# Optimization experiments

Measured on AMD Instinct MI355X. Metric: run time of the kernel, lower is better.

Reference implementation:

```python
import jax, jax.numpy as jnp
import numpy as np
from jax import lax

C = 256
POOL = 7
NUM_CLASSES = 81
D = NUM_CLASSES - 1
STRIDES = (4, 8, 16, 32)
DEC_MULT = (0.1, 0.1, 0.2, 0.2)  # decode_settings: multipliers on raw deltas
LOG_MAX = float(np.log(1000.0 / 16.0))


def setup_inputs() -> dict:
    key = jax.random.key(0)
    ks = jax.random.split(key, 16)
    n, Rp = 2, 512
    R = n * Rp
    img = 800.0
    cx = jax.random.uniform(ks[0], (R,), minval=0.0, maxval=img)
    cy = jax.random.uniform(ks[1], (R,), minval=0.0, maxval=img)
    w = jax.random.uniform(ks[2], (R,), minval=16.0, maxval=300.0)
    h = jax.random.uniform(ks[3], (R,), minval=16.0, maxval=300.0)
    x1 = jnp.clip(cx - w / 2, 0.0, img - 1.0)
    y1 = jnp.clip(cy - h / 2, 0.0, img - 1.0)
    x2 = jnp.minimum(jnp.maximum(cx + w / 2, x1 + 1.0), img)
    y2 = jnp.minimum(jnp.maximum(cy + h / 2, y1 + 1.0), img)
    proposals = jnp.stack([x1, y1, x2, y2], -1)
    imidx = jnp.repeat(jnp.arange(n, dtype=jnp.int32), Rp)
    fmaps = {}
    for li, s in enumerate(STRIDES):
        hw = int(800 // s)
        fmaps[f"fmap{li}"] = jax.random.normal(ks[4 + li], (n, hw, hw, C), jnp.float32)
    c1, clin = C * POOL * POOL, 1024
    def lin(k, fi, fo):
        return (jax.random.normal(k, (fi, fo), jnp.float32) / np.sqrt(fi).astype(np.float32),
                jnp.zeros((fo,), jnp.float32))
    W0, b0 = lin(ks[8], c1, clin)
    W1, b1 = lin(ks[9], clin, clin)
    Wc, bc = lin(ks[10], clin, NUM_CLASSES)
    Wr, br = lin(ks[11], clin, NUM_CLASSES * 4)
    imsizes = jnp.full((n, 2), img, jnp.float32)  # (h, w) per image
    return dict(proposals=proposals, imidx=imidx, **fmaps,
                W0=W0, b0=b0, W1=W1, b1=b1, Wc=Wc, bc=bc, Wr=Wr, br=br,
                imsizes=imsizes, score_thr=0.05, iou_thr=0.5, imtop=100, min_size=1.0)


def _roi_align_level(fmap, boxes, imidx, stride):
    # fmap [n,H,W,C], boxes [R,4] xyxy in image coords; 1 sample per bin, bilinear.
    n, H, W, c = fmap.shape
    s = 1.0 / stride
    x1, y1, x2, y2 = boxes[:, 0] * s, boxes[:, 1] * s, boxes[:, 2] * s, boxes[:, 3] * s
    g = (jnp.arange(POOL, dtype=jnp.float32) + 0.5) / POOL  # bin centers in [0,1]
    xs = x1[:, None] + g[None, :] * (x2 - x1)[:, None] - 0.5  # [R,POOL]
    ys = y1[:, None] + g[None, :] * (y2 - y1)[:, None] - 0.5
    R = boxes.shape[0]
    xx = jnp.broadcast_to(xs[:, None, :], (R, POOL, POOL))
    yy = jnp.broadcast_to(ys[:, :, None], (R, POOL, POOL))
    x0f, y0f = jnp.floor(xx), jnp.floor(yy)
    wx, wy = xx - x0f, yy - y0f
    x0 = jnp.clip(x0f.astype(jnp.int32), 0, W - 1)
    x1i = jnp.clip(x0f.astype(jnp.int32) + 1, 0, W - 1)
    y0 = jnp.clip(y0f.astype(jnp.int32), 0, H - 1)
    y1i = jnp.clip(y0f.astype(jnp.int32) + 1, 0, H - 1)
    ii = imidx[:, None, None]
    v00 = fmap[ii, y0, x0]; v01 = fmap[ii, y0, x1i]
    v10 = fmap[ii, y1i, x0]; v11 = fmap[ii, y1i, x1i]  # each [R,POOL,POOL,C]
    wx, wy = wx[..., None], wy[..., None]
    return (v00 * (1 - wx) * (1 - wy) + v01 * wx * (1 - wy)
            + v10 * (1 - wx) * wy + v11 * wx * wy)


def _forward(proposals, imidx, fmaps, W0, b0, W1, b1, Wc, bc, Wr, br,
             imsizes, score_thr, iou_thr, imtop, min_size):
    R = proposals.shape[0]
    pw = proposals[:, 2] - proposals[:, 0]
    ph = proposals[:, 3] - proposals[:, 1]
    # FPN level assignment (torchvision canonical formula)
    lvl = jnp.floor(4.0 + jnp.log2(jnp.sqrt(pw * ph) / 224.0 + 1e-6))
    lvl = jnp.clip(lvl, 2, 5).astype(jnp.int32) - 2
    pooled = jnp.zeros((R, POOL, POOL, C), fmaps[0].dtype)
    for k, (fm, st) in enumerate(zip(fmaps, STRIDES)):
        pk = _roi_align_level(fm, proposals, imidx, st)
        pooled = jnp.where((lvl == k)[:, None, None, None], pk, pooled)
    # two-FC head + cls/reg
    x = pooled.reshape(R, -1)
    x = jax.nn.relu(x @ W0 + b0)
    x = jax.nn.relu(x @ W1 + b1)
    reg = (x @ Wr + br).reshape(R, NUM_CLASSES, 4)[:, 1:]      # [R,D,4]
    scr = jax.nn.softmax(x @ Wc + bc, axis=-1)[:, 1:]          # [R,D]
    cls = jnp.broadcast_to(jnp.arange(1, NUM_CLASSES, dtype=jnp.int32), (R, D))
    # decode boxes (proposal cwh + weighted deltas, log-space clamp)
    cx = (proposals[:, 0] + proposals[:, 2]) * 0.5
    cy = (proposals[:, 1] + proposals[:, 3]) * 0.5
    dx = reg[..., 0] * DEC_MULT[0]
    dy = reg[..., 1] * DEC_MULT[1]
    dw = jnp.minimum(reg[..., 2] * DEC_MULT[2], LOG_MAX)
    dh = jnp.minimum(reg[..., 3] * DEC_MULT[3], LOG_MAX)
    ncx = dx * pw[:, None] + cx[:, None]
    ncy = dy * ph[:, None] + cy[:, None]
    nw = jnp.exp(dw) * pw[:, None]
    nh = jnp.exp(dh) * ph[:, None]
    hb = imsizes[imidx, 0][:, None]
    wb = imsizes[imidx, 1][:, None]
    bx1 = jnp.clip(ncx - nw / 2, 0.0, wb); bx2 = jnp.clip(ncx + nw / 2, 0.0, wb)
    by1 = jnp.clip(ncy - nh / 2, 0.0, hb); by2 = jnp.clip(ncy + nh / 2, 0.0, hb)
    boxes = jnp.stack([bx1, by1, bx2, by2], -1)                # [R,D,4]
    valid = (scr > score_thr) & (bx2 - bx1 >= min_size) & (by2 - by1 >= min_size)
    # flatten roi-class pairs; class-offset boxes = torchvision batched_nms trick
    M = R * D
    boxes_f = boxes.reshape(M, 4)
    scr_f = scr.reshape(M)
    cls_f = cls.reshape(M)
    valid_f = valid.reshape(M)
    imidx_f = jnp.repeat(imidx, D)
    off = cls_f.astype(boxes_f.dtype)[:, None] * (jnp.max(imsizes) + 2.0)
    bo = boxes_f + off
    areas = (bo[:, 2] - bo[:, 0]) * (bo[:, 3] - bo[:, 1])
    def nms(scores0):
        def step(scores, _):
            i = jnp.argmax(scores)
            s = scores[i]
            b = bo[i]
            iw = jnp.clip(jnp.minimum(b[2], bo[:, 2]) - jnp.maximum(b[0], bo[:, 0]), 0.0)
            ih = jnp.clip(jnp.minimum(b[3], bo[:, 3]) - jnp.maximum(b[1], bo[:, 1]), 0.0)
            inter = iw * ih
            iou = inter / (areas[i] + areas - inter + 1e-6)
            scores = jnp.where(iou > iou_thr, -1.0, scores)
            scores = scores.at[i].set(-1.0)
            return scores, (i, s)
        _, (idx, s) = lax.scan(step, scores0, None, length=imtop)
        return idx, s
    n = imsizes.shape[0]
    ob, osc, ocl = [], [], []
    for i in range(n):
        s0 = jnp.where(valid_f & (imidx_f == i), scr_f, -1.0)
        idx, s = nms(s0)
        keep = s > 0.0  # padded slots have score <= 0
        ob.append(jnp.where(keep[:, None], boxes_f[idx], 0.0))
        osc.append(jnp.where(keep, s, 0.0))
        ocl.append(jnp.where(keep, cls_f[idx], -1))
    return jnp.stack(ob), jnp.stack(osc), jnp.stack(ocl)


def reference(proposals, imidx, fmap0, fmap1, fmap2, fmap3, W0, b0, W1, b1,
              Wc, bc, Wr, br, imsizes, score_thr, iou_thr, imtop, min_size):
    return _forward(proposals, imidx, (fmap0, fmap1, fmap2, fmap3), W0, b0, W1,
                    b1, Wc, bc, Wr, br, imsizes, score_thr, iou_thr, int(imtop),
                    min_size)
```

## Files before the change

kernel.cpp:

```cpp
#include <hip/hip_runtime.h>
#include <math.h>

#define CCH 256
#define NPOOL 7
#define NCLS 81
#define DCLS 80
#define NHEAD 512
#define FLOG_MAX 4.1351666f

typedef _Float16 half8 __attribute__((ext_vector_type(8)));
typedef _Float16 half4 __attribute__((ext_vector_type(4)));
typedef float floatx4 __attribute__((ext_vector_type(4)));

__global__ void zero_k(float4* __restrict__ p, int count4)
{
    int i = blockIdx.x * blockDim.x + threadIdx.x;
    if (i < count4) p[i] = make_float4(0.f, 0.f, 0.f, 0.f);
}

__device__ __forceinline__ void roi_setup(
    const float* __restrict__ prop, const int* __restrict__ imidx,
    const float* __restrict__ f0, const float* __restrict__ f1,
    const float* __restrict__ f2, const float* __restrict__ f3,
    int h0, int h1, int h2, int h3, int b,
// ... 87 lines not shown
    half4 h, l;
#pragma unroll
    for (int e = 0; e < 4; ++e) {
        float v = p00[e] * w00 + p01[e] * w01 + p10[e] * w10 + p11[e] * w11;
        _Float16 hh = (_Float16)v;
        h[e] = hh;
        l[e] = (_Float16)(v - (float)hh);
    }
    size_t idx = (size_t)b * CCH + c4;
    *(half4*)(poolH + idx) = h;
    *(half4*)(poolL + idx) = l;
}

__device__ __forceinline__ void conv_fast_body(
    const float* __restrict__ W, _Float16* __restrict__ WtH,
    _Float16* __restrict__ WtL, int K, int N, int k0, int n0, int t,
    float (*sh)[65])
{
#pragma unroll
    for (int p = 0; p < 4; ++p) {
        int idx = p * 256 + t;
        int kr = idx >> 4, nc = (idx & 15) * 4;
        float4 v = *(const float4*)(W + (size_t)(k0 + kr) * N + n0 + nc);
        sh[kr][nc + 0] = v.x; sh[kr][nc + 1] = v.y;
        sh[kr][nc + 2] = v.z; sh[kr][nc + 3] = v.w;
    }
    __syncthreads();
#pragma unroll
    for (int p = 0; p < 4; ++p) {
        int idx = p * 256 + t;
        int nr = idx >> 4, kc = (idx & 15) * 4;
        half4 h, l;
#pragma unroll
        for (int i = 0; i < 4; ++i) {
            float v = sh[kc + i][nr];
            _Float16 hh = (_Float16)v;
            h[i] = hh;
            l[i] = (_Float16)(v - (float)hh);
        }
        *(half4*)(WtH + (size_t)(n0 + nr) * K + k0 + kc) = h;
        *(half4*)(WtL + (size_t)(n0 + nr) * K + k0 + kc) = l;
    }
}

__device__ __forceinline__ void conv_guard_body(
    const float* __restrict__ W, _Float16* __restrict__ WtH,
    _Float16* __restrict__ WtL, int K, int N, int Kt, int rowofs,
    int k0, int n0, int t, float (*sh)[65])
{
#pragma unroll
    for (int p = 0; p < 4; ++p) {
        int idx = p * 256 + t;
        int kr = idx >> 4, nc = (idx & 15) * 4;
#pragma unroll
        for (int e = 0; e < 4; ++e) {
            int nn = n0 + nc + e;
            sh[kr][nc + e] = (nn < N) ? W[(size_t)(k0 + kr) * N + nn] : 0.0f;
        }
    }
    __syncthreads();
#pragma unroll
    for (int p = 0; p < 4; ++p) {
        int idx = p * 256 + t;
        int nr = idx >> 4, kc = (idx & 15) * 4;
        if (n0 + nr < N) {
            half4 h, l;
#pragma unroll
            for (int i = 0; i < 4; ++i) {
                float v = sh[kc + i][nr];
                _Float16 hh = (_Float16)v;
                h[i] = hh;
                l[i] = (_Float16)(v - (float)hh);
            }
            *(half4*)(WtH + (size_t)(rowofs + n0 + nr) * Kt + k0 + kc) = h;
            *(half4*)(WtL + (size_t)(rowofs + n0 + nr) * Kt + k0 + kc) = l;
        }
    }
}

__global__ __launch_bounds__(256) void pre_uber_k(
    const float* __restrict__ prop, const int* __restrict__ imidx,
    const float* __restrict__ f0, const float* __restrict__ f1,
    const float* __restrict__ f2, const float* __restrict__ f3,
    int h0, int h1, int h2, int h3,
    _Float16* __restrict__ poolH, _Float16* __restrict__ poolL,
    const float* __restrict__ W0, _Float16* __restrict__ W0tH, _Float16* __restrict__ W0tL,
    float4* __restrict__ zp, int zc4,
    int* __restrict__ cntp, int ncnt,
    int R, int K0, int CL)
{
    __shared__ float sh[64][65];
    int b = blockIdx.x, t = threadIdx.x;

    if (blockIdx.x == 0 && t < ncnt) cntp[t] = 0;

    int NB_ROI = (R * 49) / 4;
    int KT0 = K0 / 64, NT0 = CL / 64;
    int NB_CW0 = KT0 * NT0;

    if (b < NB_ROI) {
        roi_f16v4_body(prop, imidx, f0, f1, f2, f3, h0, h1, h2, h3, b, t,
                       poolH, poolL);
        return;
    }
    b -= NB_ROI;
    if (b < NB_CW0) {
        int k0 = (b % KT0) * 64, n0 = (b / KT0) * 64;
        conv_fast_body(W0, W0tH, W0tL, K0, CL, k0, n0, t, sh);
        return;
    }
    b -= NB_CW0;
    {
        int i = b * 256 + t;
        if (i < zc4) zp[i] = make_float4(0.f, 0.f, 0.f, 0.f);
    }
}

__global__ void act_split_k(const float* __restrict__ acc,
                            const float* __restrict__ bias,
                            _Float16* __restrict__ outH,
                            _Float16* __restrict__ outL,
                            int total, int CL)
{
    int i = (blockIdx.x * blockDim.x + threadIdx.x) * 4;
    if (i >= total) return;
    int b = i % CL;
    float4 v = *(const float4*)(acc + i);
    float4 bb = *(const float4*)(bias + b);
    const float* pv = (const float*)&v;
    const float* pb = (const float*)&bb;
    half4 h, l;
#pragma unroll
    for (int e = 0; e < 4; ++e) {
        float f = fmaxf(pv[e] + pb[e], 0.0f);
        _Float16 hh = (_Float16)f;
        h[e] = hh;
        l[e] = (_Float16)(f - (float)hh);
    }
    *(half4*)(outH + i) = h;
    *(half4*)(outL + i) = l;
}

__device__ __forceinline__ void dma16(const _Float16* g, _Float16* l)
{
    __builtin_amdgcn_global_load_lds(
        (const __attribute__((address_space(1))) unsigned int*)g,
        (__attribute__((address_space(3))) unsigned int*)l, 16, 0, 0);
}

#define LDKE 32
#define DKQ_SWZ(lane)  ((((lane) & 3) ^ (((lane) >> 3) & 3)) << 3)
#define FK_SWZ(lane)   (((((lane) >> 4) ^ (((lane) >> 1) & 3))) << 3)

__global__ __launch_bounds__(256) void gemm_fc0_conv_k(
    const _Float16* __restrict__ Ah, const _Float16* __restrict__ Al,
    const _Float16* __restrict__ Bh, const _Float16* __restrict__ Bl,
    float* __restrict__ Cacc, int M, int N, int K, int Kc, int SP, int nbg,
    const float* __restrict__ W1, _Float16* __restrict__ W1tH, _Float16* __restrict__ W1tL,
    const float* __restrict__ Wc, const float* __restrict__ Wr,
    _Float16* __restrict__ WheadtH, _Float16* __restrict__ WheadtL, int CL)
{
    __shared__ __align__(16) char smem[4 * 128 * LDKE * 2];

    int t = threadIdx.x;

    if (blockIdx.x >= nbg) {
        float (*sh)[65] = (float(*)[65])smem;
        int b = blockIdx.x - nbg;
        int KT1 = CL / 64;
        int NB_CW1 = KT1 * KT1;
        int NB_CWc = KT1 * ((NCLS + 63) / 64);
        if (b < NB_CW1) {
            int k0 = (b % KT1) * 64, n0 = (b / KT1) * 64;
            conv_fast_body(W1, W1tH, W1tL, CL, CL, k0, n0, t, sh);
            return;
        }
        b -= NB_CW1;
        if (b < NB_CWc) {
            int k0 = (b % KT1) * 64, n0 = (b / KT1) * 64;
            conv_guard_body(Wc, WheadtH, WheadtL, CL, NCLS, CL, 0, k0, n0, t, sh);
            return;
        }
        b -= NB_CWc;
        {
            int k0 = (b % KT1) * 64, n0 = (b / KT1) * 64;
            conv_guard_body(Wr, WheadtH, WheadtL, CL, NCLS * 4, CL, NCLS, k0, n0, t, sh);
            return;
        }
    }

    _Float16* sAh = (_Float16*)smem;
    _Float16* sAl = sAh + 128 * LDKE;
    _Float16* sBh = sAl + 128 * LDKE;
    _Float16* sBl = sBh + 128 * LDKE;

    int bid = blockIdx.x;
    int z = bid % SP;
    int q = bid / SP;
    int NT = N >> 7;
    int nn = q % NT;
    int m = q / NT;
    int m0 = m * 128, n0 = nn * 128;
    int kb = z * Kc;
    int ke = min(K, kb + Kc);

    int lane = t & 63, w = t >> 6;
    int wr = w >> 1, wc = w & 1;
    int fr = lane & 15;
    int fk = FK_SWZ(lane);

    int drow = w * 32 + (lane >> 2);
    int dkq = DKQ_SWZ(lane);
    const _Float16* gAh = Ah + (size_t)(m0 + drow) * K + dkq;
    const _Float16* gAl = Al + (size_t)(m0 + drow) * K + dkq;
    const _Float16* gBh = Bh + (size_t)(n0 + drow) * K + dkq;
    const _Float16* gBl = Bl + (size_t)(n0 + drow) * K + dkq;
    size_t rowskip = (size_t)16 * K;

    _Float16* lAh0 = &sAh[(w * 2 + 0) * 512];
    _Float16* lAh1 = &sAh[(w * 2 + 1) * 512];
    _Float16* lAl0 = &sAl[(w * 2 + 0) * 512];
    _Float16* lAl1 = &sAl[(w * 2 + 1) * 512];
    _Float16* lBh0 = &sBh[(w * 2 + 0) * 512];
    _Float16* lBh1 = &sBh[(w * 2 + 1) * 512];
    _Float16* lBl0 = &sBl[(w * 2 + 0) * 512];
    _Float16* lBl1 = &sBl[(w * 2 + 1) * 512];

    floatx4 acc[4][4] = {};

    for (int k0 = kb; k0 < ke; k0 += 32) {
        dma16(gAh + k0, lAh0);
        dma16(gAh + rowskip + k0, lAh1);
        dma16(gAl + k0, lAl0);
        dma16(gAl + rowskip + k0, lAl1);
        dma16(gBh + k0, lBh0);
        dma16(gBh + rowskip + k0, lBh1);
        dma16(gBl + k0, lBl0);
        dma16(gBl + rowskip + k0, lBl1);
        __syncthreads();

        half8 ah[4], al[4], bh[4], bl[4];
#pragma unroll
        for (int i = 0; i < 4; ++i) {
            int ar = wr * 64 + i * 16 + fr;
            ah[i] = *(const half8*)&sAh[ar * LDKE + fk];
            al[i] = *(const half8*)&sAl[ar * LDKE + fk];
            int bc = wc * 64 + i * 16 + fr;
            bh[i] = *(const half8*)&sBh[bc * LDKE + fk];
            bl[i] = *(const half8*)&sBl[bc * LDKE + fk];
        }
#pragma unroll
        for (int i = 0; i < 4; ++i)
#pragma unroll
            for (int j = 0; j < 4; ++j) {
                acc[i][j] = __builtin_amdgcn_mfma_f32_16x16x32_f16(ah[i], bh[j], acc[i][j], 0, 0, 0);
                acc[i][j] = __builtin_amdgcn_mfma_f32_16x16x32_f16(ah[i], bl[j], acc[i][j], 0, 0, 0);
                acc[i][j] = __builtin_amdgcn_mfma_f32_16x16x32_f16(al[i], bh[j], acc[i][j], 0, 0, 0);
            }
        __syncthreads();
    }

    int rbase = (lane >> 4) * 4;
#pragma unroll
    for (int i = 0; i < 4; ++i)
#pragma unroll
        for (int j = 0; j < 4; ++j) {
            int col = n0 + wc * 64 + j * 16 + fr;
#pragma unroll
            for (int r = 0; r < 4; ++r) {
                int row = m0 + wr * 64 + i * 16 + rbase + r;
                atomicAdd(&Cacc[(size_t)row * N + col], acc[i][j][r]);
            }
        }
}

__global__ __launch_bounds__(256) void gemm_mfma_fused64_k(
    const _Float16* __restrict__ Ah, const _Float16* __restrict__ Al,
    const _Float16* __restrict__ Bh, const _Float16* __restrict__ Bl,
    const float* __restrict__ bias,
    float* __restrict__ Cout,
    _Float16* __restrict__ outH, _Float16* __restrict__ outL,
    int M, int N, int K, int mode)
{
    __shared__ _Float16 sAh[2][64 * LDKE], sAl[2][64 * LDKE];
    __shared__ _Float16 sBh[2][64 * LDKE], sBl[2][64 * LDKE];

    int m0 = blockIdx.y * 64, n0 = blockIdx.x * 64;
    int t = threadIdx.x;
    int lane = t & 63, w = t >> 6;
    int wr = w >> 1, wc = w & 1;
    int fr = lane & 15;
    int fk = FK_SWZ(lane);

    int drow = w * 16 + (lane >> 2);
    int dkq = DKQ_SWZ(lane);
    const _Float16* gAh = Ah + (size_t)(m0 + drow) * K + dkq;
    const _Float16* gAl = Al + (size_t)(m0 + drow) * K + dkq;
    const _Float16* gBh = Bh + (size_t)(n0 + drow) * K + dkq;
    const _Float16* gBl = Bl + (size_t)(n0 + drow) * K + dkq;
    int lofs = w * 512;

    int nt = K >> 5;

    dma16(gAh + 0, &sAh[0][lofs]);
    dma16(gAl + 0, &sAl[0][lofs]);
    dma16(gBh + 0, &sBh[0][lofs]);
    dma16(gBl + 0, &sBl[0][lofs]);
    __syncthreads();

    floatx4 acc[2][2] = {};

    for (int tt = 0; tt < nt; ++tt) {
        int c = tt & 1, nb = c ^ 1;
        if (tt + 1 < nt) {
            int k1 = (tt + 1) << 5;
            dma16(gAh + k1, &sAh[nb][lofs]);
            dma16(gAl + k1, &sAl[nb][lofs]);
            dma16(gBh + k1, &sBh[nb][lofs]);
            dma16(gBl + k1, &sBl[nb][lofs]);
        }

        half8 ah[2], av[2], bh[2], bv[2];
#pragma unroll
        for (int i = 0; i < 2; ++i) {
            int ar = wr * 32 + i * 16 + fr;
            ah[i] = *(const half8*)&sAh[c][ar * LDKE + fk];
            av[i] = *(const half8*)&sAl[c][ar * LDKE + fk];
            int bc = wc * 32 + i * 16 + fr;
            bh[i] = *(const half8*)&sBh[c][bc * LDKE + fk];
            bv[i] = *(const half8*)&sBl[c][bc * LDKE + fk];
        }
#pragma unroll
        for (int i = 0; i < 2; ++i)
#pragma unroll
            for (int j = 0; j < 2; ++j) {
                acc[i][j] = __builtin_amdgcn_mfma_f32_16x16x32_f16(ah[i], bh[j], acc[i][j], 0, 0, 0);
                acc[i][j] = __builtin_amdgcn_mfma_f32_16x16x32_f16(ah[i], bv[j], acc[i][j], 0, 0, 0);
                acc[i][j] = __builtin_amdgcn_mfma_f32_16x16x32_f16(av[i], bh[j], acc[i][j], 0, 0, 0);
            }
        __syncthreads();
    }

    int rbase = (lane >> 4) * 4;
#pragma unroll
    for (int i = 0; i < 2; ++i)
#pragma unroll
        for (int j = 0; j < 2; ++j) {
            int col = n0 + wc * 32 + j * 16 + fr;
#pragma unroll
            for (int r = 0; r < 4; ++r) {
                int row = m0 + wr * 32 + i * 16 + rbase + r;
                float v = acc[i][j][r];
                if (mode == 0) {
                    Cout[(size_t)row * N + col] = v;
                } else {
                    float f = fmaxf(v + bias[col], 0.0f);
                    _Float16 hh = (_Float16)f;
                    outH[(size_t)row * N + col] = hh;
                    outL[(size_t)row * N + col] = (_Float16)(f - (float)hh);
                }
            }
        }
}

__global__ __launch_bounds__(256) void gemm_splitk_k(const float* __restrict__ A,
                                                     const float* __restrict__ B,
                                                     const float* __restrict__ abias,
                                                     float* __restrict__ Cacc,
                                                     int M, int N, int K, int Kc)
{
    __shared__ float Ast[16][68];
    __shared__ float Bs[16][68];

    int m0 = blockIdx.y * 64, n0 = blockIdx.x * 64;
    int kb = blockIdx.z * Kc;
    int ke = min(K, kb + Kc);
    int tid = threadIdx.x;
    int tx = tid & 15, ty = tid >> 4;
    int arow = tid >> 2, akq = (tid & 3) << 2;
    int bcol = tid & 63, bk = tid >> 6;

    const float* Arow = A + (size_t)(m0 + arow) * K;
    bool nfull = (n0 + 64 <= N);

    float acc[4][4] = {};

    for (int k0 = kb; k0 < ke; k0 += 16) {
        float4 av = *(const float4*)(Arow + k0 + akq);
        if (abias) {
            av.x = fmaxf(av.x + abias[k0 + akq + 0], 0.0f);
            av.y = fmaxf(av.y + abias[k0 + akq + 1], 0.0f);
            av.z = fmaxf(av.z + abias[k0 + akq + 2], 0.0f);
            av.w = fmaxf(av.w + abias[k0 + akq + 3], 0.0f);
        }
        float bv[4];
        if (nfull) {
#pragma unroll
            for (int e = 0; e < 4; ++e)
                bv[e] = B[(size_t)(k0 + bk * 4 + e) * N + n0 + bcol];
        } else {
            bool ok = (n0 + bcol) < N;
#pragma unroll
            for (int e = 0; e < 4; ++e)
                bv[e] = ok ? B[(size_t)(k0 + bk * 4 + e) * N + n0 + bcol] : 0.0f;
        }
        __syncthreads();
        Ast[akq + 0][arow] = av.x;
        Ast[akq + 1][arow] = av.y;
        Ast[akq + 2][arow] = av.z;
        Ast[akq + 3][arow] = av.w;
#pragma unroll
        for (int e = 0; e < 4; ++e) Bs[bk * 4 + e][bcol] = bv[e];
        __syncthreads();

#pragma unroll
        for (int kk = 0; kk < 16; ++kk) {
            float4 af = *(const float4*)&Ast[kk][ty * 4];
            float4 bf = *(const float4*)&Bs[kk][tx * 4];
            float a_[4] = {af.x, af.y, af.z, af.w};
            float b_[4] = {bf.x, bf.y, bf.z, bf.w};
#pragma unroll
            for (int i = 0; i < 4; ++i)
#pragma unroll
                for (int j = 0; j < 4; ++j)
                    acc[i][j] = fmaf(a_[i], b_[j], acc[i][j]);
        }
    }

#pragma unroll
    for (int i = 0; i < 4; ++i) {
        int row = m0 + ty * 4 + i;
#pragma unroll
        for (int j = 0; j < 4; ++j) {
            int col = n0 + tx * 4 + j;
            if (col < N) atomicAdd(&Cacc[(size_t)row * N + col], acc[i][j]);
        }
    }
}

__global__ void softmax_k(const float* __restrict__ logits, int ldl,
                          const float* __restrict__ bc,
                          float* __restrict__ scr)
{
    int r = blockIdx.x;
    int t = threadIdx.x;
    const float* row = logits + (size_t)r * ldl;

    float v0 = row[t] + bc[t];
    float v1 = (t + 64 < NCLS) ? (row[t + 64] + bc[t + 64]) : -INFINITY;
    float m = fmaxf(v0, v1);
#pragma unroll
    for (int o = 32; o > 0; o >>= 1) m = fmaxf(m, __shfl_down(m, o));
    m = __shfl(m, 0);

    float e0 = expf(v0 - m);
    float e1 = (t + 64 < NCLS) ? expf(v1 - m) : 0.0f;
    float sum = e0 + e1;
#pragma unroll
    for (int o = 32; o > 0; o >>= 1) sum += __shfl_down(sum, o);
    sum = __shfl(sum, 0);
    float inv = 1.0f / sum;

    if (t >= 1)        scr[(size_t)r * DCLS + (t - 1)]  = e0 * inv;
    if (t + 64 < NCLS) scr[(size_t)r * DCLS + (t + 63)] = e1 * inv;
}

__global__ __launch_bounds__(256) void compact_k(
    const float* __restrict__ head, int ldh, int regofs,
    const float* __restrict__ bc,
    const float* __restrict__ br,
    const float* __restrict__ prop,
    const int* __restrict__ imidx,
    const float* __restrict__ imsz,
    const float* __restrict__ score_thr_p,
    const float* __restrict__ min_size_p,
    int* __restrict__ cntp,
    int* __restrict__ cidx,
    float* __restrict__ cscore,
    float* __restrict__ cbo,
    float* __restrict__ cbox,
    float* __restrict__ carea,
    int M, int n, int R)
{
    int wid = threadIdx.x >> 6, t = threadIdx.x & 63;
    int r = blockIdx.x * 4 + wid;
    if (r >= R) return;

    const float* row = head + (size_t)r * ldh;
    float v0 = row[t] + bc[t];
    float v1 = (t + 64 < NCLS) ? (row[t + 64] + bc[t + 64]) : -INFINITY;
    float m = fmaxf(v0, v1);
#pragma unroll
    for (int o = 32; o > 0; o >>= 1) m = fmaxf(m, __shfl_down(m, o));
    m = __shfl(m, 0);

    float e0 = expf(v0 - m);
    float e1 = (t + 64 < NCLS) ? expf(v1 - m) : 0.0f;
    float sum = e0 + e1;
#pragma unroll
    for (int o = 32; o > 0; o >>= 1) sum += __shfl_down(sum, o);
    sum = __shfl(sum, 0);
    float inv = 1.0f / sum;

    float score_thr = score_thr_p[0];
    float min_size  = min_size_p[0];
    float immax = imsz[0];
    for (int q = 1; q < 2 * n; ++q) immax = fmaxf(immax, imsz[q]);

    int img = imidx[r];
    int base = img * M;
    const float* pr = prop + (size_t)r * 4;
    float pw = pr[2] - pr[0], ph = pr[3] - pr[1];
    float cx = (pr[0] + pr[2]) * 0.5f, cy = (pr[1] + pr[3]) * 0.5f;
// ... 314 lines not shown
        float bx1 = fminf(fmaxf(ncx - nw * 0.5f, 0.0f), wbound);
        float bx2 = fminf(fmaxf(ncx + nw * 0.5f, 0.0f), wbound);
        float by1 = fminf(fmaxf(ncy - nh * 0.5f, 0.0f), hbound);
        float by2 = fminf(fmaxf(ncy + nh * 0.5f, 0.0f), hbound);
        if (bx2 - bx1 < min_size || by2 - by1 < min_size) continue;

        float off = (float)cls * (immax + 2.0f);
        int p = atomicAdd(&cnt, 1);
        cidx[base + p] = j;
        cscore[base + p] = s;
        cbox[(size_t)(base + p) * 4 + 0] = bx1;
        cbox[(size_t)(base + p) * 4 + 1] = by1;
        cbox[(size_t)(base + p) * 4 + 2] = bx2;
        cbox[(size_t)(base + p) * 4 + 3] = by2;
        cbo[(size_t)(base + p) * 4 + 0] = bx1 + off;
        cbo[(size_t)(base + p) * 4 + 1] = by1 + off;
        cbo[(size_t)(base + p) * 4 + 2] = bx2 + off;
        cbo[(size_t)(base + p) * 4 + 3] = by2 + off;
        carea[base + p] = (bx2 - bx1) * (by2 - by1);
    }
    __syncthreads();
    int K = cnt;

    float* ob  = out;
    float* osc = out + (size_t)n * imtop * 4;
    float* ocl = out + (size_t)n * imtop * 5;

    int it = 0;
    for (; it < imtop; ++it) {
        float best = -1e30f; int bg = 0x7fffffff; int bl = -1;
        for (int p = t; p < K; p += T) {
            float sv = cscore[base + p];
            int g = cidx[base + p];
            if (sv > best || (sv == best && g < bg)) { best = sv; bg = g; bl = p; }
        }
#pragma unroll
        for (int o = 32; o > 0; o >>= 1) {
            float os = __shfl_down(best, o);
            int   og = __shfl_down(bg, o);
            int   ol = __shfl_down(bl, o);
            if (os > best || (os == best && og < bg)) { best = os; bg = og; bl = ol; }
        }
        if (lane == 0) { ws_sc[wid] = best; ws_g[wid] = bg; ws_p[wid] = bl; }
        __syncthreads();
        if (wid == 0) {
            float b2 = (lane < NW) ? ws_sc[lane] : -1e30f;
            int   g2 = (lane < NW) ? ws_g[lane] : 0x7fffffff;
            int   l2 = (lane < NW) ? ws_p[lane] : -1;
#pragma unroll
            for (int o = NW / 2; o > 0; o >>= 1) {
                float os = __shfl_down(b2, o);
                int   og = __shfl_down(g2, o);
                int   ol = __shfl_down(l2, o);
                if (os > b2 || (os == b2 && og < g2)) { b2 = os; g2 = og; l2 = ol; }
            }
            if (lane == 0) {
                f_sc = b2;
                if (b2 > 0.0f) {
                    int lp = l2;
                    size_t oslot = (size_t)img * imtop + it;
                    ob[oslot * 4 + 0] = cbox[(size_t)(base + lp) * 4 + 0];
                    ob[oslot * 4 + 1] = cbox[(size_t)(base + lp) * 4 + 1];
                    ob[oslot * 4 + 2] = cbox[(size_t)(base + lp) * 4 + 2];
                    ob[oslot * 4 + 3] = cbox[(size_t)(base + lp) * 4 + 3];
                    osc[oslot] = b2;
                    ocl[oslot] = (float)(g2 % DCLS + 1);
                    f_o0 = cbo[(size_t)(base + lp) * 4 + 0];
                    f_o1 = cbo[(size_t)(base + lp) * 4 + 1];
                    f_o2 = cbo[(size_t)(base + lp) * 4 + 2];
                    f_o3 = cbo[(size_t)(base + lp) * 4 + 3];
                    f_ar = carea[base + lp];
                    cscore[base + lp] = -1.0f;
                }
            }
        }
        __syncthreads();
        if (f_sc <= 0.0f) break;

        float b0 = f_o0, b1 = f_o1, b2_ = f_o2, b3 = f_o3, ai = f_ar;
        for (int p = t; p < K; p += T) {
            float c0 = cbo[(size_t)(base + p) * 4 + 0];
            float c1 = cbo[(size_t)(base + p) * 4 + 1];
            float c2 = cbo[(size_t)(base + p) * 4 + 2];
            float c3 = cbo[(size_t)(base + p) * 4 + 3];
            float iw = fmaxf(fminf(b2_, c2) - fmaxf(b0, c0), 0.0f);
            float ih = fmaxf(fminf(b3, c3) - fmaxf(b1, c1), 0.0f);
            float inter = iw * ih;
            float iou = inter / (ai + carea[base + p] - inter + 1e-6f);
            if (iou > iou_thr) cscore[base + p] = -1.0f;
        }
        __syncthreads();
    }

    for (int q = it + t; q < imtop; q += T) {
        size_t oslot = (size_t)img * imtop + q;
        ob[oslot * 4 + 0] = 0.0f;
        ob[oslot * 4 + 1] = 0.0f;
        ob[oslot * 4 + 2] = 0.0f;
        ob[oslot * 4 + 3] = 0.0f;
        osc[oslot] = 0.0f;
        ocl[oslot] = -1.0f;
    }
}

extern "C" void kernel_launch(void* const* d_in, const int* in_sizes, int n_in,
                              void* d_out, int out_size, void* d_ws, size_t ws_size,
                              hipStream_t stream)
{
    const float* prop   = (const float*)d_in[0];
    const int*   imidx  = (const int*)d_in[1];
    const float* f0     = (const float*)d_in[2];
    const float* f1     = (const float*)d_in[3];
    const float* f2     = (const float*)d_in[4];
    const float* f3     = (const float*)d_in[5];
    const float* W0     = (const float*)d_in[6];
    const float* b0     = (const float*)d_in[7];
    const float* W1     = (const float*)d_in[8];
    const float* b1     = (const float*)d_in[9];
    const float* Wc     = (const float*)d_in[10];
    const float* bc     = (const float*)d_in[11];
    const float* Wr     = (const float*)d_in[12];
    const float* br     = (const float*)d_in[13];
    const float* imsz   = (const float*)d_in[14];
    const float* sthr   = (const float*)d_in[15];
    const float* ithr   = (const float*)d_in[16];
    const float* msz    = (const float*)d_in[18];

    int R = in_sizes[1];
    int n = in_sizes[14] / 2;
    int imtop = out_size / (n * 6);
    int M = R * DCLS;
    int K0 = NPOOL * NPOOL * CCH;
    int CL = in_sizes[7];

    int h0 = (int)(sqrtf((float)(in_sizes[2] / (n * CCH))) + 0.5f);
    int h1 = (int)(sqrtf((float)(in_sizes[3] / (n * CCH))) + 0.5f);
    int h2 = (int)(sqrtf((float)(in_sizes[4] / (n * CCH))) + 0.5f);
    int h3 = (int)(sqrtf((float)(in_sizes[5] / (n * CCH))) + 0.5f);

    float* outf = (float*)d_out;

    size_t szPool  = (size_t)R * K0 * 2;
    size_t szX     = (size_t)R * CL * 4;
    size_t szHead  = (size_t)R * NHEAD * 4;
    size_t szWh    = (size_t)NHEAD * CL * 2;
    size_t szXh    = (size_t)R * CL * 2;
    size_t szW1t   = (size_t)CL * CL * 2;
    size_t szScr   = (size_t)R * DCLS * 4;

    size_t needed = 4 * szPool + 2 * szX + szHead + 2 * szWh
                  + 4 * szXh + 2 * szW1t + szScr;

    int splitK0 = 8;
    bool mfma_ok = (ws_size >= needed) && (R % 128 == 0) && (CL % 128 == 0)
                 && (K0 % (splitK0 * 32) == 0) && (CL % 32 == 0)
                 && ((R * 49) % 4 == 0) && (K0 % 64 == 0) && (CL % 64 == 0)
                 && (R % 4 == 0);

    if (mfma_ok) {
        uint8_t* w = (uint8_t*)d_ws;
        size_t o = 0;
        _Float16* poolH   = (_Float16*)(w + o); o += szPool;
        _Float16* poolL   = (_Float16*)(w + o); o += szPool;
        _Float16* W0tH    = (_Float16*)(w + o); o += szPool;
        _Float16* W0tL    = (_Float16*)(w + o); o += szPool;
        float*    x0acc   = (float*)(w + o);    o += szX;
        float*    unused  = (float*)(w + o);    o += szX;
        float*    headacc = (float*)(w + o);    o += szHead;
        _Float16* WheadtH = (_Float16*)(w + o); o += szWh;
        _Float16* WheadtL = (_Float16*)(w + o); o += szWh;
        _Float16* x0H     = (_Float16*)(w + o); o += szXh;
        _Float16* x0L     = (_Float16*)(w + o); o += szXh;
        _Float16* x1H     = (_Float16*)(w + o); o += szXh;
        _Float16* x1L     = (_Float16*)(w + o); o += szXh;
        _Float16* W1tH    = (_Float16*)(w + o); o += szW1t;
        _Float16* W1tL    = (_Float16*)(w + o); o += szW1t;
        float*    scr     = (float*)(w + o);
        (void)unused;

        int* cnt = (int*)scr;

        int*   cidx   = (int*)d_ws;
        float* cscore = (float*)(cidx + (size_t)n * M);
        float* cbo    = cscore + (size_t)n * M;
        float* cbox   = cbo + (size_t)n * M * 4;
        float* carea  = cbox + (size_t)n * M * 4;

        {
            int NB_ROI = (R * 49) / 4;
            int NB_CW0 = (K0 / 64) * (CL / 64);
            int zc4    = (int)(szX / 16);
            int NB_Z   = (zc4 + 255) / 256;
            int NB = NB_ROI + NB_CW0 + NB_Z;
            pre_uber_k<<<dim3(NB), dim3(256), 0, stream>>>(
                prop, imidx, f0, f1, f2, f3, h0, h1, h2, h3,
                poolH, poolL,
                W0, W0tH, W0tL,
                (float4*)x0acc, zc4,
                cnt, n,
                R, K0, CL);
        }
        {
            int nbg = splitK0 * (R / 128) * (CL / 128);
            int KT1 = CL / 64;
            int NB_CW1 = KT1 * KT1;
            int NB_CWc = KT1 * ((NCLS + 63) / 64);
            int NB_CWr = KT1 * ((NCLS * 4 + 63) / 64);
            gemm_fc0_conv_k<<<dim3(nbg + NB_CW1 + NB_CWc + NB_CWr), dim3(256), 0, stream>>>(
                poolH, poolL, W0tH, W0tL, x0acc, R, CL, K0, K0 / splitK0, splitK0, nbg,
                W1, W1tH, W1tL, Wc, Wr, WheadtH, WheadtL, CL);
        }
        act_split_k<<<dim3((R * CL / 4 + 255) / 256), dim3(256), 0, stream>>>(
            x0acc, b0, x0H, x0L, R * CL, CL);
        gemm_mfma_fused64_k<<<dim3(CL / 64, R / 64), dim3(256), 0, stream>>>(
            x0H, x0L, W1tH, W1tL, b1, nullptr, x1H, x1L, R, CL, CL, 1);
        gemm_mfma_fused64_k<<<dim3(NHEAD / 64, R / 64), dim3(256), 0, stream>>>(
            x1H, x1L, WheadtH, WheadtL, nullptr, headacc, nullptr, nullptr, R, NHEAD, CL, 0);
        compact_k<<<dim3(R / 4), dim3(256), 0, stream>>>(
            headacc, NHEAD, NCLS, bc, br, prop, imidx, imsz, sthr, msz,
            cnt, cidx, cscore, cbo, cbox, carea, M, n, R);
        nms_pick_k<<<dim3(n), dim3(NMS_T), 0, stream>>>(
            ithr, cnt, cidx, cscore, cbo, cbox, carea, outf, M, n, imtop);
    } else {
        float* ws = (float*)d_ws;
        size_t off = 0;
        float* pooled  = ws + off; off += (size_t)R * K0;
        float* x0acc   = ws + off; off += (size_t)R * CL;
        float* x1acc   = ws + off; off += (size_t)R * CL;
        float* logits  = ws + off; off += (size_t)R * NCLS;
        off = (off + 3) & ~(size_t)3;
        float* reg     = ws + off; off += (size_t)R * NCLS * 4;
        float* scr     = ws + off; off += (size_t)R * DCLS;

        int*   cidx   = (int*)ws;
        float* cscore = (float*)(cidx + (size_t)n * M);
        float* cbo    = cscore + (size_t)n * M;
        float* cbox   = cbo + (size_t)n * M * 4;
        float* carea  = cbox + (size_t)n * M * 4;

        {
            size_t zcount = (size_t)(reg + (size_t)R * NCLS * 4 - x0acc);
            int c4 = (int)(zcount / 4);
            zero_k<<<dim3((c4 + 255) / 256), dim3(256), 0, stream>>>((float4*)x0acc, c4);
        }
        roi_align_k<<<dim3(R * 49), dim3(256), 0, stream>>>(
            prop, imidx, f0, f1, f2, f3, h0, h1, h2, h3, pooled);
        gemm_splitk_k<<<dim3(CL / 64, R / 64, 8), dim3(256), 0, stream>>>(
            pooled, W0, nullptr, x0acc, R, CL, K0, 1568);
        gemm_splitk_k<<<dim3(CL / 64, R / 64, 4), dim3(256), 0, stream>>>(
            x0acc, W1, b0, x1acc, R, CL, CL, 256);
        gemm_splitk_k<<<dim3((NCLS + 63) / 64, R / 64, 8), dim3(256), 0, stream>>>(
            x1acc, Wc, b1, logits, R, NCLS, CL, 128);
        gemm_splitk_k<<<dim3((NCLS * 4 + 63) / 64, R / 64, 4), dim3(256), 0, stream>>>(
            x1acc, Wr, b1, reg, R, NCLS * 4, CL, 256);
        softmax_k<<<dim3(R), dim3(64), 0, stream>>>(logits, NCLS, bc, scr);
        nms_k<<<dim3(n), dim3(NMS_T), 0, stream>>>(
            scr, prop, imidx, reg, NCLS * 4, 0, br, imsz, sthr, msz, ithr,
            cidx, cscore, cbo, cbox, carea, outf, M, n, imtop);
    }
}
```

Baseline: 378.1 us.

## Replace 64x64 fused GEMMs for fc1 and head with 128x128 split-K atomic GEMMs

The fc1 and head GEMMs previously ran on a double-buffered 64x64-tile MFMA kernel with the bias and ReLU epilogue fused in. They now use a 128x128-tile split-K kernel that accumulates into zeroed fp32 buffers with atomics, and fc1's bias, ReLU and fp16 hi/lo split moves into a separate act_split_k launch. The pre-kernel zeroing range grows to cover the new accumulators. The aim is larger tiles and more blocks along K for these small GEMMs, at the cost of atomic traffic, an extra kernel launch and a single-buffered load loop with no prefetch.

```diff
diff --git a/kernel.cpp b/kernel.cpp
--- a/kernel.cpp
+++ b/kernel.cpp
@@ -263,6 +263,95 @@
 #define DKQ_SWZ(lane)  ((((lane) & 3) ^ (((lane) >> 3) & 3)) << 3)
 #define FK_SWZ(lane)   (((((lane) >> 4) ^ (((lane) >> 1) & 3))) << 3)
 
+__global__ __launch_bounds__(256) void gemm_mfma_split_k(
+    const _Float16* __restrict__ Ah, const _Float16* __restrict__ Al,
+    const _Float16* __restrict__ Bh, const _Float16* __restrict__ Bl,
+    float* __restrict__ Cacc, int M, int N, int K, int Kc, int SP)
+{
+    __shared__ _Float16 sAh[128 * LDKE], sAl[128 * LDKE];
+    __shared__ _Float16 sBh[128 * LDKE], sBl[128 * LDKE];
+
+    int bid = blockIdx.x;
+    int z = bid % SP;
+    int q = bid / SP;
+    int NT = N >> 7;
+    int nn = q % NT;
+    int m = q / NT;
+    int m0 = m * 128, n0 = nn * 128;
+    int kb = z * Kc;
+    int ke = min(K, kb + Kc);
+
+    int t = threadIdx.x;
+    int lane = t & 63, w = t >> 6;
+    int wr = w >> 1, wc = w & 1;
+    int fr = lane & 15;
+    int fk = FK_SWZ(lane);
+
+    int drow = w * 32 + (lane >> 2);
+    int dkq = DKQ_SWZ(lane);
+    const _Float16* gAh = Ah + (size_t)(m0 + drow) * K + dkq;
+    const _Float16* gAl = Al + (size_t)(m0 + drow) * K + dkq;
+    const _Float16* gBh = Bh + (size_t)(n0 + drow) * K + dkq;
+    const _Float16* gBl = Bl + (size_t)(n0 + drow) * K + dkq;
+    size_t rowskip = (size_t)16 * K;
+
+    _Float16* lAh0 = &sAh[(w * 2 + 0) * 512];
+    _Float16* lAh1 = &sAh[(w * 2 + 1) * 512];
+    _Float16* lAl0 = &sAl[(w * 2 + 0) * 512];
+    _Float16* lAl1 = &sAl[(w * 2 + 1) * 512];
+    _Float16* lBh0 = &sBh[(w * 2 + 0) * 512];
+    _Float16* lBh1 = &sBh[(w * 2 + 1) * 512];
+    _Float16* lBl0 = &sBl[(w * 2 + 0) * 512];
+    _Float16* lBl1 = &sBl[(w * 2 + 1) * 512];
+
+    floatx4 acc[4][4] = {};
+
+    for (int k0 = kb; k0 < ke; k0 += 32) {
+        dma16(gAh + k0, lAh0);
+        dma16(gAh + rowskip + k0, lAh1);
+        dma16(gAl + k0, lAl0);
+        dma16(gAl + rowskip + k0, lAl1);
+        dma16(gBh + k0, lBh0);
+        dma16(gBh + rowskip + k0, lBh1);
+        dma16(gBl + k0, lBl0);
+        dma16(gBl + rowskip + k0, lBl1);
+        __syncthreads();
+
+        half8 ah[4], al[4], bh[4], bl[4];
+#pragma unroll
+        for (int i = 0; i < 4; ++i) {
+            int ar = wr * 64 + i * 16 + fr;
+            ah[i] = *(const half8*)&sAh[ar * LDKE + fk];
+            al[i] = *(const half8*)&sAl[ar * LDKE + fk];
+            int bc = wc * 64 + i * 16 + fr;
+            bh[i] = *(const half8*)&sBh[bc * LDKE + fk];
+            bl[i] = *(const half8*)&sBl[bc * LDKE + fk];
+        }
+#pragma unroll
+        for (int i = 0; i < 4; ++i)
+#pragma unroll
+            for (int j = 0; j < 4; ++j) {
+                acc[i][j] = __builtin_amdgcn_mfma_f32_16x16x32_f16(ah[i], bh[j], acc[i][j], 0, 0, 0);
+                acc[i][j] = __builtin_amdgcn_mfma_f32_16x16x32_f16(ah[i], bl[j], acc[i][j], 0, 0, 0);
+                acc[i][j] = __builtin_amdgcn_mfma_f32_16x16x32_f16(al[i], bh[j], acc[i][j], 0, 0, 0);
+            }
+        __syncthreads();
+    }
+
+    int rbase = (lane >> 4) * 4;
+#pragma unroll
+    for (int i = 0; i < 4; ++i)
+#pragma unroll
+        for (int j = 0; j < 4; ++j) {
+            int col = n0 + wc * 64 + j * 16 + fr;
+#pragma unroll
+            for (int r = 0; r < 4; ++r) {
+                int row = m0 + wr * 64 + i * 16 + rbase + r;
+                atomicAdd(&Cacc[(size_t)row * N + col], acc[i][j][r]);
+            }
+        }
+}
+
 __global__ __launch_bounds__(256) void gemm_fc0_conv_k(
     const _Float16* __restrict__ Ah, const _Float16* __restrict__ Al,
     const _Float16* __restrict__ Bh, const _Float16* __restrict__ Bl,
@@ -381,95 +470,6 @@
             for (int r = 0; r < 4; ++r) {
                 int row = m0 + wr * 64 + i * 16 + rbase + r;
                 atomicAdd(&Cacc[(size_t)row * N + col], acc[i][j][r]);
-            }
-        }
-}
-
-__global__ __launch_bounds__(256) void gemm_mfma_fused64_k(
-    const _Float16* __restrict__ Ah, const _Float16* __restrict__ Al,
-    const _Float16* __restrict__ Bh, const _Float16* __restrict__ Bl,
-    const float* __restrict__ bias,
-    float* __restrict__ Cout,
-    _Float16* __restrict__ outH, _Float16* __restrict__ outL,
-    int M, int N, int K, int mode)
-{
-    __shared__ _Float16 sAh[2][64 * LDKE], sAl[2][64 * LDKE];
-    __shared__ _Float16 sBh[2][64 * LDKE], sBl[2][64 * LDKE];
-
-    int m0 = blockIdx.y * 64, n0 = blockIdx.x * 64;
-    int t = threadIdx.x;
-    int lane = t & 63, w = t >> 6;
-    int wr = w >> 1, wc = w & 1;
-    int fr = lane & 15;
-    int fk = FK_SWZ(lane);
-
-    int drow = w * 16 + (lane >> 2);
-    int dkq = DKQ_SWZ(lane);
-    const _Float16* gAh = Ah + (size_t)(m0 + drow) * K + dkq;
-    const _Float16* gAl = Al + (size_t)(m0 + drow) * K + dkq;
-    const _Float16* gBh = Bh + (size_t)(n0 + drow) * K + dkq;
-    const _Float16* gBl = Bl + (size_t)(n0 + drow) * K + dkq;
-    int lofs = w * 512;
-
-    int nt = K >> 5;
-
-    dma16(gAh + 0, &sAh[0][lofs]);
-    dma16(gAl + 0, &sAl[0][lofs]);
-    dma16(gBh + 0, &sBh[0][lofs]);
-    dma16(gBl + 0, &sBl[0][lofs]);
-    __syncthreads();
-
-    floatx4 acc[2][2] = {};
-
-    for (int tt = 0; tt < nt; ++tt) {
-        int c = tt & 1, nb = c ^ 1;
-        if (tt + 1 < nt) {
-            int k1 = (tt + 1) << 5;
-            dma16(gAh + k1, &sAh[nb][lofs]);
-            dma16(gAl + k1, &sAl[nb][lofs]);
-            dma16(gBh + k1, &sBh[nb][lofs]);
-            dma16(gBl + k1, &sBl[nb][lofs]);
-        }
-
-        half8 ah[2], av[2], bh[2], bv[2];
-#pragma unroll
-        for (int i = 0; i < 2; ++i) {
-            int ar = wr * 32 + i * 16 + fr;
-            ah[i] = *(const half8*)&sAh[c][ar * LDKE + fk];
-            av[i] = *(const half8*)&sAl[c][ar * LDKE + fk];
-            int bc = wc * 32 + i * 16 + fr;
-            bh[i] = *(const half8*)&sBh[c][bc * LDKE + fk];
-            bv[i] = *(const half8*)&sBl[c][bc * LDKE + fk];
-        }
-#pragma unroll
-        for (int i = 0; i < 2; ++i)
-#pragma unroll
-            for (int j = 0; j < 2; ++j) {
-                acc[i][j] = __builtin_amdgcn_mfma_f32_16x16x32_f16(ah[i], bh[j], acc[i][j], 0, 0, 0);
-                acc[i][j] = __builtin_amdgcn_mfma_f32_16x16x32_f16(ah[i], bv[j], acc[i][j], 0, 0, 0);
-                acc[i][j] = __builtin_amdgcn_mfma_f32_16x16x32_f16(av[i], bh[j], acc[i][j], 0, 0, 0);
-            }
-        __syncthreads();
-    }
-
-    int rbase = (lane >> 4) * 4;
-#pragma unroll
-    for (int i = 0; i < 2; ++i)
-#pragma unroll
-        for (int j = 0; j < 2; ++j) {
-            int col = n0 + wc * 32 + j * 16 + fr;
-#pragma unroll
-            for (int r = 0; r < 4; ++r) {
-                int row = m0 + wr * 32 + i * 16 + rbase + r;
-                float v = acc[i][j][r];
-                if (mode == 0) {
-                    Cout[(size_t)row * N + col] = v;
-                } else {
-                    float f = fmaxf(v + bias[col], 0.0f);
-                    _Float16 hh = (_Float16)f;
-                    outH[(size_t)row * N + col] = hh;
-                    outL[(size_t)row * N + col] = (_Float16)(f - (float)hh);
-                }
             }
         }
 }
@@ -1090,8 +1090,11 @@
                   + 4 * szXh + 2 * szW1t + szScr;
 
     int splitK0 = 8;
+    const int SP1 = 4;
+    const int SP2 = 8;
     bool mfma_ok = (ws_size >= needed) && (R % 128 == 0) && (CL % 128 == 0)
-                 && (K0 % (splitK0 * 32) == 0) && (CL % 32 == 0)
+                 && (K0 % (splitK0 * 32) == 0) && (CL % (SP1 * 32) == 0)
+                 && (CL % (SP2 * 32) == 0) && (NHEAD % 128 == 0)
                  && ((R * 49) % 4 == 0) && (K0 % 64 == 0) && (CL % 64 == 0)
                  && (R % 4 == 0);
 
@@ -1103,7 +1106,7 @@
         _Float16* W0tH    = (_Float16*)(w + o); o += szPool;
         _Float16* W0tL    = (_Float16*)(w + o); o += szPool;
         float*    x0acc   = (float*)(w + o);    o += szX;
-        float*    unused  = (float*)(w + o);    o += szX;
+        float*    x1acc   = (float*)(w + o);    o += szX;
         float*    headacc = (float*)(w + o);    o += szHead;
         _Float16* WheadtH = (_Float16*)(w + o); o += szWh;
         _Float16* WheadtL = (_Float16*)(w + o); o += szWh;
@@ -1114,8 +1117,6 @@
         _Float16* W1tH    = (_Float16*)(w + o); o += szW1t;
         _Float16* W1tL    = (_Float16*)(w + o); o += szW1t;
         float*    scr     = (float*)(w + o);
-        (void)unused;
-
         int* cnt = (int*)scr;
 
         int*   cidx   = (int*)d_ws;
@@ -1127,7 +1128,7 @@
         {
             int NB_ROI = (R * 49) / 4;
             int NB_CW0 = (K0 / 64) * (CL / 64);
-            int zc4    = (int)(szX / 16);
+            int zc4    = (int)((2 * szX + szHead) / 16);
             int NB_Z   = (zc4 + 255) / 256;
             int NB = NB_ROI + NB_CW0 + NB_Z;
             pre_uber_k<<<dim3(NB), dim3(256), 0, stream>>>(
@@ -1150,10 +1151,12 @@
         }
         act_split_k<<<dim3((R * CL / 4 + 255) / 256), dim3(256), 0, stream>>>(
             x0acc, b0, x0H, x0L, R * CL, CL);
-        gemm_mfma_fused64_k<<<dim3(CL / 64, R / 64), dim3(256), 0, stream>>>(
-            x0H, x0L, W1tH, W1tL, b1, nullptr, x1H, x1L, R, CL, CL, 1);
-        gemm_mfma_fused64_k<<<dim3(NHEAD / 64, R / 64), dim3(256), 0, stream>>>(
-            x1H, x1L, WheadtH, WheadtL, nullptr, headacc, nullptr, nullptr, R, NHEAD, CL, 0);
+        gemm_mfma_split_k<<<dim3(SP1 * (R / 128) * (CL / 128)), dim3(256), 0, stream>>>(
+            x0H, x0L, W1tH, W1tL, x1acc, R, CL, CL, CL / SP1, SP1);
+        act_split_k<<<dim3((R * CL / 4 + 255) / 256), dim3(256), 0, stream>>>(
+            x1acc, b1, x1H, x1L, R * CL, CL);
+        gemm_mfma_split_k<<<dim3(SP2 * (R / 128) * (NHEAD / 128)), dim3(256), 0, stream>>>(
+            x1H, x1L, WheadtH, WheadtL, headacc, R, NHEAD, CL, CL / SP2, SP2);
         compact_k<<<dim3(R / 4), dim3(256), 0, stream>>>(
             headacc, NHEAD, NCLS, bc, br, prop, imidx, imsz, sthr, msz,
             cnt, cidx, cscore, cbo, cbox, carea, M, n, R);
```

Result: no change. 378.6 us (+0.1%).
